# Kernel optimization log

Hardware: AMD Instinct MI355X
Metric: run time of the kernel (lower is better)

## Reference

```python
import jax, jax.numpy as jnp
import numpy as np

B, T, D, H, L, V = 16, 1024, 512, 8, 6, 96
HS = D // H
FF = 4 * D


def setup_inputs() -> dict:
    key = jax.random.key(0)
    ks = jax.random.split(key, 16)
    n = lambda k, shape: jax.random.normal(k, shape, jnp.float32) * 0.02
    return {
        "idx": jax.random.randint(ks[0], (B, T), 0, V),
        "targets": jax.random.randint(ks[1], (B, T), 0, V),
        "tok_emb": n(ks[2], (V, D)),
        "pos_emb": n(ks[3], (T, D)),
        "Wq": n(ks[4], (L, H, D, HS)),
        "Wk": n(ks[5], (L, H, D, HS)),
        "Wv": n(ks[6], (L, H, D, HS)),
        "Wproj": n(ks[7], (L, D, D)),
        "bproj": jnp.zeros((L, D), jnp.float32),
        "W1": n(ks[8], (L, D, FF)),
        "b1": jnp.zeros((L, FF), jnp.float32),
        "W2": n(ks[9], (L, FF, D)),
        "b2": jnp.zeros((L, D), jnp.float32),
        "ln1_s": jnp.ones((L, D), jnp.float32),
        "ln1_b": jnp.zeros((L, D), jnp.float32),
        "ln2_s": jnp.ones((L, D), jnp.float32),
        "ln2_b": jnp.zeros((L, D), jnp.float32),
        "lnf_s": jnp.ones((D,), jnp.float32),
        "lnf_b": jnp.zeros((D,), jnp.float32),
        "Wout": n(ks[10], (D, V)),
        "bout": jnp.zeros((V,), jnp.float32),
    }


def _ln(x, s, b, eps=1e-5):
    m = x.mean(-1, keepdims=True)
    v = ((x - m) ** 2).mean(-1, keepdims=True)
    return (x - m) * jax.lax.rsqrt(v + eps) * s + b


def reference(idx, targets, tok_emb, pos_emb, Wq, Wk, Wv, Wproj, bproj,
              W1, b1, W2, b2, ln1_s, ln1_b, ln2_s, ln2_b, lnf_s, lnf_b,
              Wout, bout):
    x = tok_emb[idx] + pos_emb[:T]  # [B,T,D]
    causal = jnp.tril(jnp.ones((T, T), jnp.bool_))
    scale = D ** (-0.5)  # NOTE: source scales by full channel dim, not head_size
    for l in range(L):
        h = _ln(x, ln1_s[l], ln1_b[l])
        q = jnp.einsum("btd,hdk->bhtk", h, Wq[l])
        k = jnp.einsum("btd,hdk->bhtk", h, Wk[l])
        v = jnp.einsum("btd,hdk->bhtk", h, Wv[l])
        att = jnp.einsum("bhtk,bhsk->bhts", q, k) * scale
        att = jnp.where(causal, att, -jnp.inf)
        att = jax.nn.softmax(att, axis=-1)
        o = jnp.einsum("bhts,bhsk->bhtk", att, v)
        o = o.transpose(0, 2, 1, 3).reshape(B, T, D)  # concat heads
        x = x + (o @ Wproj[l] + bproj[l])
        h2 = _ln(x, ln2_s[l], ln2_b[l])
        x = x + (jnp.maximum(h2 @ W1[l] + b1[l], 0.0) @ W2[l] + b2[l])
    x = _ln(x, lnf_s, lnf_b)
    logits = (x @ Wout + bout).reshape(B * T, V)
    logp = jax.nn.log_softmax(logits, axis=-1)
    loss = -logp[jnp.arange(B * T), targets.reshape(-1)].mean()
    return logits, loss
```

## Files before the change

kernel.cpp:

```cpp
#include <hip/hip_runtime.h>

#define B_  16
#define T_  1024
#define D_  512
#define H_  8
#define L_  6
#define V_  96
#define HS_ 64
#define FF_ 2048
#define BT_ (B_*T_)

typedef __attribute__((ext_vector_type(8))) short bf16x8;
typedef __attribute__((ext_vector_type(4))) float f32x4;

typedef __attribute__((address_space(3))) unsigned int lds_u32_t;
typedef const __attribute__((address_space(1))) unsigned int glb_u32_t;

__device__ __forceinline__ void gload16(const unsigned short* g, unsigned short* l) {
  __builtin_amdgcn_global_load_lds((glb_u32_t*)g, (lds_u32_t*)l, 16, 0, 0);
}

__device__ __forceinline__ unsigned short f2b(float f) {
  unsigned u = __float_as_uint(f);
  unsigned r = (u + 0x7FFFu + ((u >> 16) & 1u)) >> 16;
  return (unsigned short)r;
}

__global__ void zero_kernel(float* p) { p[0] = 0.f; }

__global__ __launch_bounds__(128) void embed_kernel(const int* __restrict__ idx,
    const float* __restrict__ tok, const float* __restrict__ pos, float* __restrict__ x) {
  int bt = blockIdx.x;
  int t  = bt & (T_ - 1);
  int id = idx[bt];
  if (id < 0) id = 0; if (id > V_ - 1) id = V_ - 1;
  int d  = threadIdx.x * 4;
  float4 tv = *(const float4*)(tok + (size_t)id * D_ + d);
  float4 pv = *(const float4*)(pos + (size_t)t  * D_ + d);
  float4 o = {tv.x + pv.x, tv.y + pv.y, tv.z + pv.z, tv.w + pv.w};
  *(float4*)(x + (size_t)bt * D_ + d) = o;
}

__global__ __launch_bounds__(256) void transpose_cvt(const float* __restrict__ src,
    unsigned short* __restrict__ dst, int R, int C, long sstride, long dstride) {
  __shared__ float t[32][33];
  const float* s = src + (size_t)blockIdx.z * sstride;
  unsigned short* d = dst + (size_t)blockIdx.z * dstride;
  int r0 = blockIdx.y * 32, c0 = blockIdx.x * 32;
  int tr = threadIdx.x >> 5, tc = threadIdx.x & 31;
#pragma unroll
  for (int i = 0; i < 4; ++i)
    t[tr + i * 8][tc] = s[(size_t)(r0 + tr + i * 8) * C + c0 + tc];
  __syncthreads();
#pragma unroll
  for (int i = 0; i < 4; ++i)
    d[(size_t)(c0 + tr + i * 8) * R + r0 + tc] = f2b(t[tc][tr + i * 8]);
}

template<bool BF16OUT>
__global__ __launch_bounds__(256) void ln_kernel(const float* __restrict__ x,
    const float* __restrict__ s, const float* __restrict__ b, void* __restrict__ outv) {
  int wave = threadIdx.x >> 6;
  int lane = threadIdx.x & 63;
  int r = blockIdx.x * 4 + wave;
  const float* xr = x + (size_t)r * D_;
  float vals[8];
  float sum = 0.f;
#pragma unroll
  for (int j = 0; j < 8; ++j) { vals[j] = xr[j * 64 + lane]; sum += vals[j]; }
#pragma unroll
  for (int o = 32; o > 0; o >>= 1) sum += __shfl_xor(sum, o, 64);
  float mean = sum * (1.f / D_);
  float vs = 0.f;
#pragma unroll
  for (int j = 0; j < 8; ++j) { float d = vals[j] - mean; vs += d * d; }
#pragma unroll
  for (int o = 32; o > 0; o >>= 1) vs += __shfl_xor(vs, o, 64);
  float rstd = rsqrtf(vs * (1.f / D_) + 1e-5f);
#pragma unroll
  for (int j = 0; j < 8; ++j) {
    int c = j * 64 + lane;
    float v = (vals[j] - mean) * rstd * s[c] + b[c];
    if (BF16OUT) ((unsigned short*)outv)[(size_t)r * D_ + c] = f2b(v);
    else         ((float*)outv)[(size_t)r * D_ + c] = v;
  }
}

#define BK 32
template<bool ACC, bool RELU, bool BIAS, int OUTMODE>
__global__ __launch_bounds__(256) void mfma_gemm(
    const unsigned short* __restrict__ A,
    const unsigned short* __restrict__ Bt,
    const float* __restrict__ bias,
    void* __restrict__ Cv,
    int K, int ldc) {
  __shared__ unsigned short Al[128 * BK];
  __shared__ unsigned short Bl[128 * BK];
  const int m0 = blockIdx.x * 128, n0 = blockIdx.y * 128;
  const int tid = threadIdx.x;
  const int lane = tid & 63, wave = tid >> 6;
  const int wy = wave >> 1, wx = wave & 1;
  const int l15 = lane & 15, quad = lane >> 4;

  const int sbase = wave * 1024;
  const int soff  = sbase + lane * 16;
  const int r0 = soff >> 6, c0e = (soff & 63) >> 1;
  const int r1 = r0 + 64;
  const unsigned short* gA0 = A  + (size_t)(m0 + r0) * K + c0e;
  const unsigned short* gA1 = A  + (size_t)(m0 + r1) * K + c0e;
  const unsigned short* gB0 = Bt + (size_t)(n0 + r0) * K + c0e;
  const unsigned short* gB1 = Bt + (size_t)(n0 + r1) * K + c0e;
  unsigned short* lA0 = &Al[sbase >> 1];
  unsigned short* lA1 = &Al[(sbase + 4096) >> 1];
  unsigned short* lB0 = &Bl[sbase >> 1];
  unsigned short* lB1 = &Bl[(sbase + 4096) >> 1];

  f32x4 acc[4][4];
  const f32x4 z4 = {0.f, 0.f, 0.f, 0.f};
#pragma unroll
  for (int mi = 0; mi < 4; ++mi)
#pragma unroll
    for (int ni = 0; ni < 4; ++ni) acc[mi][ni] = z4;

  for (int k0 = 0; k0 < K; k0 += BK) {
    gload16(gA0 + k0, lA0);
    gload16(gA1 + k0, lA1);
    gload16(gB0 + k0, lB0);
    gload16(gB1 + k0, lB1);
    __syncthreads();
    bf16x8 af[4], bfr[4];
#pragma unroll
    for (int mi = 0; mi < 4; ++mi)
      af[mi] = *(const bf16x8*)(&Al[(wy * 64 + mi * 16 + l15) * BK + quad * 8]);
#pragma unroll
    for (int ni = 0; ni < 4; ++ni)
      bfr[ni] = *(const bf16x8*)(&Bl[(wx * 64 + ni * 16 + l15) * BK + quad * 8]);
#pragma unroll
    for (int mi = 0; mi < 4; ++mi)
#pragma unroll
      for (int ni = 0; ni < 4; ++ni)
        acc[mi][ni] = __builtin_amdgcn_mfma_f32_16x16x32_bf16(af[mi], bfr[ni], acc[mi][ni], 0, 0, 0);
    __syncthreads();
  }
#pragma unroll
  for (int mi = 0; mi < 4; ++mi) {
    int row0 = m0 + wy * 64 + mi * 16 + quad * 4;
#pragma unroll
    for (int ni = 0; ni < 4; ++ni) {
      int col = n0 + wx * 64 + ni * 16 + l15;
      float bb = BIAS ? bias[col] : 0.f;
#pragma unroll
      for (int r = 0; r < 4; ++r) {
        float v = acc[mi][ni][r] + bb;
        if (RELU) v = fmaxf(v, 0.f);
        int row = row0 + r;
        if (OUTMODE == 2) {
          int b = row >> 10, t = row & (T_ - 1);
          int h = col >> 6, hs = col & 63;
          ((unsigned short*)Cv)[((size_t)((b * H_ + h) * HS_ + hs)) * T_ + t] = f2b(v);
        } else {
          size_t off = (size_t)row * ldc + col;
          if (ACC) v += ((const float*)Cv)[off];
          if (OUTMODE == 1) ((unsigned short*)Cv)[off] = f2b(v);
          else              ((float*)Cv)[off] = v;
        }
      }
    }
  }
}

#define PSTR 72
__global__ __launch_bounds__(256) void attn_mfma(const unsigned short* __restrict__ q,
    const unsigned short* __restrict__ k, const unsigned short* __restrict__ vt,
    unsigned short* __restrict__ o) {
  __shared__ unsigned short Pbuf[2][64 * PSTR];
  const int qt = (gridDim.x - 1) - blockIdx.x;
  const int bh = blockIdx.y;
  const int b = bh >> 3, hh = bh & 7;
  const int tid = threadIdx.x;
  const int lane = tid & 63, w = tid >> 6;
  const int l15 = lane & 15, quad = lane >> 4;
  const float CEXP = 0.044194173824159216f * 1.4426950408889634f;

  bf16x8 qf[4][2];
#pragma unroll
  for (int mi = 0; mi < 4; ++mi)
#pragma unroll
    for (int c = 0; c < 2; ++c)
      qf[mi][c] = *(const bf16x8*)(q + (size_t)(b * T_ + qt * 64 + mi * 16 + l15) * D_
                                     + hh * HS_ + c * 32 + quad * 8);

  const short one_bf = (short)0x3F80;
  bf16x8 ones = {one_bf, one_bf, one_bf, one_bf, one_bf, one_bf, one_bf, one_bf};

  f32x4 oacc[4], lacc[4];
  const f32x4 z4 = {0.f, 0.f, 0.f, 0.f};
#pragma unroll
  for (int mi = 0; mi < 4; ++mi) { oacc[mi] = z4; lacc[mi] = z4; }

  for (int kt = 0; kt <= qt; ++kt) {
    f32x4 s[4];
#pragma unroll
    for (int mi = 0; mi < 4; ++mi) s[mi] = z4;
#pragma unroll
    for (int c = 0; c < 2; ++c) {
      bf16x8 kf = *(const bf16x8*)(k + (size_t)(b * T_ + kt * 64 + w * 16 + l15) * D_
                                     + hh * HS_ + c * 32 + quad * 8);
#pragma unroll
      for (int mi = 0; mi < 4; ++mi)
        s[mi] = __builtin_amdgcn_mfma_f32_16x16x32_bf16(qf[mi][c], kf, s[mi], 0, 0, 0);
    }
    unsigned short* pb = Pbuf[kt & 1];
    if (kt == qt) {
#pragma unroll
      for (int mi = 0; mi < 4; ++mi)
#pragma unroll
        for (int r = 0; r < 4; ++r) {
          int row = mi * 16 + quad * 4 + r;
          int gc = w * 16 + l15;
          float p = (gc > row) ? 0.f : exp2f(s[mi][r] * CEXP);
          pb[row * PSTR + gc] = f2b(p);
        }
    } else {
#pragma unroll
      for (int mi = 0; mi < 4; ++mi)
#pragma unroll
        for (int r = 0; r < 4; ++r) {
          int row = mi * 16 + quad * 4 + r;
          pb[row * PSTR + w * 16 + l15] = f2b(exp2f(s[mi][r] * CEXP));
        }
    }
    __syncthreads();
#pragma unroll
    for (int c = 0; c < 2; ++c) {
      bf16x8 vf = *(const bf16x8*)(vt + ((size_t)(bh * HS_ + w * 16 + l15)) * T_
                                      + kt * 64 + c * 32 + quad * 8);
#pragma unroll
      for (int mi = 0; mi < 4; ++mi) {
        bf16x8 pf = *(const bf16x8*)(&pb[(mi * 16 + l15) * PSTR + c * 32 + quad * 8]);
        oacc[mi] = __builtin_amdgcn_mfma_f32_16x16x32_bf16(pf, vf, oacc[mi], 0, 0, 0);
        lacc[mi] = __builtin_amdgcn_mfma_f32_16x16x32_bf16(pf, ones, lacc[mi], 0, 0, 0);
      }
    }
  }
#pragma unroll
  for (int mi = 0; mi < 4; ++mi)
#pragma unroll
    for (int r = 0; r < 4; ++r) {
      int row = mi * 16 + quad * 4 + r;
      float inv = 1.f / lacc[mi][r];
      o[(size_t)(b * T_ + qt * 64 + row) * D_ + hh * HS_ + w * 16 + l15] =
          f2b(oacc[mi][r] * inv);
    }
}

__global__ __launch_bounds__(256) void gemm_f32_kernel(const float* __restrict__ A, int lda,
    const float* __restrict__ Bw, int ldb, const float* __restrict__ bias,
    float* __restrict__ C, int ldc, int K, int N) {
  __shared__ float As[16][64];
  __shared__ float Bs[16][64];
  int n0 = blockIdx.y * 64;
  int nv = N - n0; if (nv > 64) nv = 64;
  int m0 = blockIdx.x * 64;
  const int tid = threadIdx.x;
  const int tx = tid & 15, ty = tid >> 4;
  const int amm = tid >> 2;
  const int akk = (tid & 3) * 4;
  const int bkk = tid >> 4;
  const int bnn = (tid & 15) * 4;
  float acc[4][4] = {};
  for (int k0 = 0; k0 < K; k0 += 16) {
    float4 av = *(const float4*)(A + (size_t)(m0 + amm) * lda + k0 + akk);
    As[akk + 0][amm] = av.x; As[akk + 1][amm] = av.y;
    As[akk + 2][amm] = av.z; As[akk + 3][amm] = av.w;
    if (bnn < nv) {
      float4 bv = *(const float4*)(Bw + (size_t)(k0 + bkk) * ldb + n0 + bnn);
      Bs[bkk][bnn + 0] = bv.x; Bs[bkk][bnn + 1] = bv.y;
      Bs[bkk][bnn + 2] = bv.z; Bs[bkk][bnn + 3] = bv.w;
    } else {
      Bs[bkk][bnn + 0] = 0.f; Bs[bkk][bnn + 1] = 0.f;
      Bs[bkk][bnn + 2] = 0.f; Bs[bkk][bnn + 3] = 0.f;
    }
    __syncthreads();
#pragma unroll
    for (int kk = 0; kk < 16; ++kk) {
      float4 a4 = *(const float4*)(&As[kk][ty * 4]);
      float4 b4 = *(const float4*)(&Bs[kk][tx * 4]);
      float aa[4] = {a4.x, a4.y, a4.z, a4.w};
      float bb[4] = {b4.x, b4.y, b4.z, b4.w};
#pragma unroll
      for (int i = 0; i < 4; ++i)
#pragma unroll
        for (int j = 0; j < 4; ++j)
          acc[i][j] = fmaf(aa[i], bb[j], acc[i][j]);
    }
    __syncthreads();
  }
  if (tx * 4 < nv) {
#pragma unroll
    for (int i = 0; i < 4; ++i) {
      float* cp = C + (size_t)(m0 + ty * 4 + i) * ldc + n0 + tx * 4;
      float4 st = {acc[i][0] + bias[n0 + tx * 4 + 0], acc[i][1] + bias[n0 + tx * 4 + 1],
                   acc[i][2] + bias[n0 + tx * 4 + 2], acc[i][3] + bias[n0 + tx * 4 + 3]};
      *(float4*)cp = st;
    }
  }
}

__global__ __launch_bounds__(256) void loss_kernel(const float* __restrict__ logits,
    const int* __restrict__ targets, float* __restrict__ loss_acc) {
  __shared__ float wsum[4];
  int wave = threadIdx.x >> 6, lane = threadIdx.x & 63;
  float local = 0.f;
  for (int r = blockIdx.x * 4 + wave; r < BT_; r += gridDim.x * 4) {
    const float* lr = logits + (size_t)r * V_;
    float v0 = lr[lane];
    float v1 = (lane < 32) ? lr[64 + lane] : -INFINITY;
    float mx = fmaxf(v0, v1);
#pragma unroll
    for (int o = 32; o > 0; o >>= 1) mx = fmaxf(mx, __shfl_xor(mx, o, 64));
    float se = expf(v0 - mx) + ((lane < 32) ? expf(v1 - mx) : 0.f);
#pragma unroll
    for (int o = 32; o > 0; o >>= 1) se += __shfl_xor(se, o, 64);
    if (lane == 0) {
      int tg = targets[r];
      if (tg < 0) tg = 0; if (tg > V_ - 1) tg = V_ - 1;
      local += (mx + logf(se)) - lr[tg];
    }
  }
  if (lane == 0) wsum[wave] = local;
  __syncthreads();
  if (threadIdx.x == 0)
    atomicAdd(loss_acc, wsum[0] + wsum[1] + wsum[2] + wsum[3]);
}

__global__ void loss_finalize_kernel(const float* __restrict__ acc, float* __restrict__ out) {
  out[(size_t)BT_ * V_] = acc[0] * (1.f / BT_);
}

static void* g_ws_fallback = nullptr;

extern "C" void kernel_launch(void* const* d_in, const int* in_sizes, int n_in,
                              void* d_out, int out_size, void* d_ws, size_t ws_size,
                              hipStream_t stream) {
  const int*   idx     = (const int*)d_in[0];
  const int*   targets = (const int*)d_in[1];
  const float* tok  = (const float*)d_in[2];
  const float* pos  = (const float*)d_in[3];
  const float* Wq   = (const float*)d_in[4];
  const float* Wk   = (const float*)d_in[5];
  const float* Wv   = (const float*)d_in[6];
  const float* Wp   = (const float*)d_in[7];
  const float* bp   = (const float*)d_in[8];
  const float* W1   = (const float*)d_in[9];
  const float* b1   = (const float*)d_in[10];
  const float* W2   = (const float*)d_in[11];
  const float* b2   = (const float*)d_in[12];
  const float* l1s  = (const float*)d_in[13];
  const float* l1b  = (const float*)d_in[14];
  const float* l2s  = (const float*)d_in[15];
  const float* l2b  = (const float*)d_in[16];
  const float* lfs  = (const float*)d_in[17];
  const float* lfb  = (const float*)d_in[18];
  const float* Wout = (const float*)d_in[19];
  const float* bout = (const float*)d_in[20];
  float* out = (float*)d_out;

  const size_t n_x  = (size_t)BT_ * D_;
  const size_t n_wT = 9437184;
  const size_t need_floats = n_x + n_x + n_x / 2 + n_x / 2 + n_x / 2 +
                             (size_t)BT_ * FF_ / 2 + n_wT + 256;
  const size_t need_bytes  = need_floats * sizeof(float);

  float* ws;
  if (ws_size >= need_bytes) {
    ws = (float*)d_ws;
  } else {
    if (!g_ws_fallback) (void)hipMalloc(&g_ws_fallback, need_bytes);
    ws = (float*)g_ws_fallback;
  }

  size_t off = 0;
  float* x  = ws + off; off += n_x;
  float* qf32 = ws + off; off += n_x;
  unsigned short* qb = (unsigned short*)qf32;
  unsigned short* kb  = (unsigned short*)(ws + off); off += n_x / 2;
  unsigned short* vtb = (unsigned short*)(ws + off); off += n_x / 2;
  unsigned short* hb  = (unsigned short*)(ws + off); off += n_x / 2;
  unsigned short* ffb = (unsigned short*)(ws + off); off += (size_t)BT_ * FF_ / 2;
  unsigned short* wqT = (unsigned short*)(ws + off);
  unsigned short* wkT = wqT + (size_t)L_ * D_ * D_;
  unsigned short* wvT = wkT + (size_t)L_ * D_ * D_;
  unsigned short* wpT = wvT + (size_t)L_ * D_ * D_;
  unsigned short* w1T = wpT + (size_t)L_ * D_ * D_;
  unsigned short* w2T = w1T + (size_t)L_ * D_ * FF_;
  off += n_wT;
  float* lacc = ws + off;

  zero_kernel<<<1, 1, 0, stream>>>(lacc);
  embed_kernel<<<BT_, 128, 0, stream>>>(idx, tok, pos, x);

  transpose_cvt<<<dim3(2, 16, 48), 256, 0, stream>>>(Wq, wqT, 512, 64, 32768, 32768);
  transpose_cvt<<<dim3(2, 16, 48), 256, 0, stream>>>(Wk, wkT, 512, 64, 32768, 32768);
  transpose_cvt<<<dim3(2, 16, 48), 256, 0, stream>>>(Wv, wvT, 512, 64, 32768, 32768);
  transpose_cvt<<<dim3(16, 16, 6), 256, 0, stream>>>(Wp, wpT, 512, 512, 262144, 262144);
  transpose_cvt<<<dim3(64, 16, 6), 256, 0, stream>>>(W1, w1T, 512, 2048, 1048576, 1048576);
  transpose_cvt<<<dim3(16, 64, 6), 256, 0, stream>>>(W2, w2T, 2048, 512, 1048576, 1048576);

  const dim3 gD(BT_ / 128, D_ / 128);
  const dim3 gF(BT_ / 128, FF_ / 128);

  for (int l = 0; l < L_; ++l) {
    ln_kernel<true><<<BT_ / 4, 256, 0, stream>>>(x, l1s + (size_t)l * D_, l1b + (size_t)l * D_, hb);
    mfma_gemm<false, false, false, 1><<<gD, 256, 0, stream>>>(
        hb, wqT + (size_t)l * D_ * D_, nullptr, qb, D_, D_);
    mfma_gemm<false, false, false, 1><<<gD, 256, 0, stream>>>(
        hb, wkT + (size_t)l * D_ * D_, nullptr, kb, D_, D_);
    mfma_gemm<false, false, false, 2><<<gD, 256, 0, stream>>>(
        hb, wvT + (size_t)l * D_ * D_, nullptr, vtb, D_, D_);
    attn_mfma<<<dim3(T_ / 64, B_ * H_), 256, 0, stream>>>(qb, kb, vtb, hb);
    mfma_gemm<true, false, true, 0><<<gD, 256, 0, stream>>>(
        hb, wpT + (size_t)l * D_ * D_, bp + (size_t)l * D_, x, D_, D_);
    ln_kernel<true><<<BT_ / 4, 256, 0, stream>>>(x, l2s + (size_t)l * D_, l2b + (size_t)l * D_, hb);
    mfma_gemm<false, true, true, 1><<<gF, 256, 0, stream>>>(
        hb, w1T + (size_t)l * D_ * FF_, b1 + (size_t)l * FF_, ffb, D_, FF_);
    mfma_gemm<true, false, true, 0><<<gD, 256, 0, stream>>>(
        ffb, w2T + (size_t)l * FF_ * D_, b2 + (size_t)l * D_, x, FF_, D_);
  }

  ln_kernel<false><<<BT_ / 4, 256, 0, stream>>>(x, lfs, lfb, qf32);
  gemm_f32_kernel<<<dim3(BT_ / 64, 2), 256, 0, stream>>>(
      qf32, D_, Wout, V_, bout, out, V_, D_, V_);
  loss_kernel<<<64, 256, 0, stream>>>(out, targets, lacc);
  loss_finalize_kernel<<<1, 1, 0, stream>>>(lacc, out);
}
```

Baseline: 2.188 ms.

## Prefetch K/V tiles and replace ones-MFMA row sums with register accumulation

In the attention kernel, the K and V fragments for the next key tile are loaded one iteration ahead to hide global-memory latency. The row-sum MFMA against a vector of ones is removed. Each lane now adds its rounded bf16 probabilities in registers, and the per-wave partials are combined with shuffles and an LDS reduction at the end. MFMA sections are wrapped in s_setprio, which adds register pressure and one extra barrier at the end.

```diff
diff --git a/kernel.cpp b/kernel.cpp
--- a/kernel.cpp
+++ b/kernel.cpp
@@ -174,6 +174,7 @@
     const unsigned short* __restrict__ k, const unsigned short* __restrict__ vt,
     unsigned short* __restrict__ o) {
   __shared__ unsigned short Pbuf[2][64 * PSTR];
+  __shared__ float Lsum[4][64];
   const int qt = (gridDim.x - 1) - blockIdx.x;
   const int bh = blockIdx.y;
   const int b = bh >> 3, hh = bh & 7;
@@ -190,26 +191,48 @@
       qf[mi][c] = *(const bf16x8*)(q + (size_t)(b * T_ + qt * 64 + mi * 16 + l15) * D_
                                      + hh * HS_ + c * 32 + quad * 8);
 
-  const short one_bf = (short)0x3F80;
-  bf16x8 ones = {one_bf, one_bf, one_bf, one_bf, one_bf, one_bf, one_bf, one_bf};
-
-  f32x4 oacc[4], lacc[4];
+  f32x4 oacc[4];
+  float psum[4][4];
   const f32x4 z4 = {0.f, 0.f, 0.f, 0.f};
 #pragma unroll
-  for (int mi = 0; mi < 4; ++mi) { oacc[mi] = z4; lacc[mi] = z4; }
+  for (int mi = 0; mi < 4; ++mi) {
+    oacc[mi] = z4;
+#pragma unroll
+    for (int r = 0; r < 4; ++r) psum[mi][r] = 0.f;
+  }
+
+  const unsigned short* kbase = k  + (size_t)(b * T_ + w * 16 + l15) * D_ + hh * HS_ + quad * 8;
+  const unsigned short* vbase = vt + ((size_t)(bh * HS_ + w * 16 + l15)) * T_ + quad * 8;
+
+  bf16x8 kf[2], vf[2];
+#pragma unroll
+  for (int c = 0; c < 2; ++c) {
+    kf[c] = *(const bf16x8*)(kbase + c * 32);
+    vf[c] = *(const bf16x8*)(vbase + c * 32);
+  }
+
+  const int gc = w * 16 + l15;
 
   for (int kt = 0; kt <= qt; ++kt) {
+    const int ktn = (kt < qt) ? kt + 1 : qt;
+    bf16x8 kfn[2], vfn[2];
+#pragma unroll
+    for (int c = 0; c < 2; ++c) {
+      kfn[c] = *(const bf16x8*)(kbase + (size_t)ktn * 64 * D_ + c * 32);
+      vfn[c] = *(const bf16x8*)(vbase + ktn * 64 + c * 32);
+    }
+
     f32x4 s[4];
 #pragma unroll
     for (int mi = 0; mi < 4; ++mi) s[mi] = z4;
-#pragma unroll
-    for (int c = 0; c < 2; ++c) {
-      bf16x8 kf = *(const bf16x8*)(k + (size_t)(b * T_ + kt * 64 + w * 16 + l15) * D_
-                                     + hh * HS_ + c * 32 + quad * 8);
+    __builtin_amdgcn_s_setprio(1);
+#pragma unroll
+    for (int c = 0; c < 2; ++c)
 #pragma unroll
       for (int mi = 0; mi < 4; ++mi)
-        s[mi] = __builtin_amdgcn_mfma_f32_16x16x32_bf16(qf[mi][c], kf, s[mi], 0, 0, 0);
-    }
+        s[mi] = __builtin_amdgcn_mfma_f32_16x16x32_bf16(qf[mi][c], kf[c], s[mi], 0, 0, 0);
+    __builtin_amdgcn_s_setprio(0);
+
     unsigned short* pb = Pbuf[kt & 1];
     if (kt == qt) {
 #pragma unroll
@@ -217,9 +240,10 @@
 #pragma unroll
         for (int r = 0; r < 4; ++r) {
           int row = mi * 16 + quad * 4 + r;
-          int gc = w * 16 + l15;
           float p = (gc > row) ? 0.f : exp2f(s[mi][r] * CEXP);
-          pb[row * PSTR + gc] = f2b(p);
+          unsigned short us = f2b(p);
+          psum[mi][r] += __uint_as_float((unsigned)us << 16);
+          pb[row * PSTR + gc] = us;
         }
     } else {
 #pragma unroll
@@ -227,28 +251,49 @@
 #pragma unroll
         for (int r = 0; r < 4; ++r) {
           int row = mi * 16 + quad * 4 + r;
-          pb[row * PSTR + w * 16 + l15] = f2b(exp2f(s[mi][r] * CEXP));
+          float p = exp2f(s[mi][r] * CEXP);
+          unsigned short us = f2b(p);
+          psum[mi][r] += __uint_as_float((unsigned)us << 16);
+          pb[row * PSTR + gc] = us;
         }
     }
     __syncthreads();
+    __builtin_amdgcn_s_setprio(1);
 #pragma unroll
     for (int c = 0; c < 2; ++c) {
-      bf16x8 vf = *(const bf16x8*)(vt + ((size_t)(bh * HS_ + w * 16 + l15)) * T_
-                                      + kt * 64 + c * 32 + quad * 8);
 #pragma unroll
       for (int mi = 0; mi < 4; ++mi) {
         bf16x8 pf = *(const bf16x8*)(&pb[(mi * 16 + l15) * PSTR + c * 32 + quad * 8]);
-        oacc[mi] = __builtin_amdgcn_mfma_f32_16x16x32_bf16(pf, vf, oacc[mi], 0, 0, 0);
-        lacc[mi] = __builtin_amdgcn_mfma_f32_16x16x32_bf16(pf, ones, lacc[mi], 0, 0, 0);
+        oacc[mi] = __builtin_amdgcn_mfma_f32_16x16x32_bf16(pf, vf[c], oacc[mi], 0, 0, 0);
       }
     }
-  }
+    __builtin_amdgcn_s_setprio(0);
+#pragma unroll
+    for (int c = 0; c < 2; ++c) { kf[c] = kfn[c]; vf[c] = vfn[c]; }
+  }
+
+#pragma unroll
+  for (int mi = 0; mi < 4; ++mi)
+#pragma unroll
+    for (int r = 0; r < 4; ++r) {
+#pragma unroll
+      for (int off = 1; off < 16; off <<= 1)
+        psum[mi][r] += __shfl_xor(psum[mi][r], off, 64);
+    }
+  if (l15 == 0) {
+#pragma unroll
+    for (int mi = 0; mi < 4; ++mi)
+#pragma unroll
+      for (int r = 0; r < 4; ++r)
+        Lsum[w][mi * 16 + quad * 4 + r] = psum[mi][r];
+  }
+  __syncthreads();
 #pragma unroll
   for (int mi = 0; mi < 4; ++mi)
 #pragma unroll
     for (int r = 0; r < 4; ++r) {
       int row = mi * 16 + quad * 4 + r;
-      float inv = 1.f / lacc[mi][r];
+      float inv = 1.f / (Lsum[0][row] + Lsum[1][row] + Lsum[2][row] + Lsum[3][row]);
       o[(size_t)(b * T_ + qt * 64 + row) * D_ + hh * HS_ + w * 16 + l15] =
           f2b(oacc[mi][r] * inv);
     }
```

After: 2.136 ms. 2.4% less time.
